# Kernel optimization log

Hardware: AMD Instinct MI355X
Metric: run time of the kernel (lower is better)

Reference implementation:

```python
import jax, jax.numpy as jnp
import numpy as np


def setup_inputs() -> dict:
    key = jax.random.key(0)
    ks = jax.random.split(key, 4)
    B, L, E = 2, 2048, 512
    scale = 0.02
    return {
        "x": jax.random.normal(ks[0], (B, L, E), dtype=jnp.float32),
        "Wq": jax.random.normal(ks[1], (E, E), dtype=jnp.float32) * scale,
        "bq": jnp.zeros((E,), dtype=jnp.float32),
        "Wk": jax.random.normal(ks[2], (E, E), dtype=jnp.float32) * scale,
        "bk": jnp.zeros((E,), dtype=jnp.float32),
        "Wv": jax.random.normal(ks[3], (E, E), dtype=jnp.float32) * scale,
        "bv": jnp.zeros((E,), dtype=jnp.float32),
        "window_size": 64,
    }


def reference(x, Wq, bq, Wk, bk, Wv, bv, window_size):
    # x: [B, L, E]; Linear weights stored torch-style as [out, in].
    B, L, E = x.shape
    q = jnp.einsum("ble,fe->blf", x, Wq) + bq  # [B, L, E]
    k = jnp.einsum("ble,fe->blf", x, Wk) + bk
    v = jnp.einsum("ble,fe->blf", x, Wv) + bv

    w = window_size
    W = 2 * w + 1
    # Window indices per query position i: [i-w, i+w], clipped; invalid masked.
    offsets = jnp.arange(-w, w + 1)                 # [W]
    idx = jnp.arange(L)[:, None] + offsets[None, :]  # [L, W]
    valid = (idx >= 0) & (idx < L)                   # [L, W]
    idx_c = jnp.clip(idx, 0, L - 1)

    k_win = k[:, idx_c]  # [B, L, W, E]
    v_win = v[:, idx_c]  # [B, L, W, E]

    scores = jnp.einsum("ble,blwe->blw", q, k_win) / jnp.sqrt(jnp.float32(E))
    scores = jnp.where(valid[None, :, :], scores, -jnp.inf)
    probs = jax.nn.softmax(scores, axis=-1)          # [B, L, W]
    out = jnp.einsum("blw,blwe->ble", probs, v_win)  # [B, L, E]
    return out
```

## Files before the change

kernel.cpp:

```cpp
#include <hip/hip_runtime.h>
#include <cstdint>
#include <cstddef>

#define L_SEQ 2048
#define E_DIM 512
#define B_SZ 2
#define WIN 64
#define SCALE_QK 0.044194173824159216f

typedef __attribute__((ext_vector_type(8))) short short8;
typedef __attribute__((ext_vector_type(4))) float floatx4;

__device__ __forceinline__ unsigned short f2bf(float f) {
    unsigned int u = __float_as_uint(f);
    u += 0x7FFFu + ((u >> 16) & 1u);
    return (unsigned short)(u >> 16);
}

__device__ __forceinline__ uint4 pk8(const float4 lo, const float4 hi) {
    uint4 r;
    asm("v_cvt_pk_bf16_f32 %0, %1, %2" : "=v"(r.x) : "v"(lo.x), "v"(lo.y));
    asm("v_cvt_pk_bf16_f32 %0, %1, %2" : "=v"(r.y) : "v"(lo.z), "v"(lo.w));
    asm("v_cvt_pk_bf16_f32 %0, %1, %2" : "=v"(r.z) : "v"(hi.x), "v"(hi.y));
    asm("v_cvt_pk_bf16_f32 %0, %1, %2" : "=v"(r.w) : "v"(hi.z), "v"(hi.w));
    return r;
}

__device__ __forceinline__ void ld16cvt(const float* g, uint4& r0, uint4& r1) {
    float4 f0 = *(const float4*)(g);
    float4 f1 = *(const float4*)(g + 4);
    float4 f2 = *(const float4*)(g + 8);
    float4 f3 = *(const float4*)(g + 12);
    r0 = pk8(f0, f1);
    r1 = pk8(f2, f3);
}

#define ALD 72
__global__ __launch_bounds__(256, 2) void qkv_fused(
    const float* __restrict__ x,
    const float* __restrict__ Wq, const float* __restrict__ Wk, const float* __restrict__ Wv,
    const float* __restrict__ bq, const float* __restrict__ bk, const float* __restrict__ bv,
    unsigned short* __restrict__ q, unsigned short* __restrict__ k,
    unsigned short* __restrict__ vt)
{
    __shared__ __align__(16) unsigned short As[64 * ALD];
    __shared__ __align__(16) unsigned short Bs[3][64 * ALD];

    const int t = threadIdx.x;
    const int w = t >> 6, l = t & 63;
    const int m0 = blockIdx.x * 64, n0 = blockIdx.y * 64;
    const float* Ws[3] = { Wq, Wk, Wv };

    floatx4 acc[3][2][2] = {};
    const int wm = (w >> 1) * 32, wn = (w & 1) * 32;
    const int fr = l & 15, fq = l >> 4, fk = fq * 8;

    const int srow = t >> 2, scol = (t & 3) * 16;
    const float* gA = x + (size_t)(m0 + srow) * 512 + scol;

    float bv_[3][2];
    {
        const float* bs[3] = { bq, bk, bv };
#pragma unroll
        for (int z = 0; z < 3; z++)
#pragma unroll
            for (int j = 0; j < 2; j++) bv_[z][j] = bs[z][n0 + wn + j * 16 + fr];
    }

    for (int kt = 0; kt < 8; kt++) {
        const int kk = kt * 64;
        uint4 r0, r1;
        ld16cvt(gA + kk, r0, r1);
        *(uint4*)&As[srow * ALD + scol]     = r0;
        *(uint4*)&As[srow * ALD + scol + 8] = r1;
#pragma unroll
        for (int z = 0; z < 3; z++) {
            ld16cvt(Ws[z] + (size_t)(n0 + srow) * 512 + scol + kk, r0, r1);
            *(uint4*)&Bs[z][srow * ALD + scol]     = r0;
            *(uint4*)&Bs[z][srow * ALD + scol + 8] = r1;
        }
        __syncthreads();

        short8 a[2][2];
#pragma unroll
        for (int i = 0; i < 2; i++)
#pragma unroll
            for (int kh = 0; kh < 2; kh++)
                a[i][kh] = *(const short8*)&As[(wm + i * 16 + fr) * ALD + kh * 32 + fk];
#pragma unroll
        for (int z = 0; z < 3; z++) {
            short8 bf[2][2];
#pragma unroll
            for (int j = 0; j < 2; j++)
#pragma unroll
                for (int kh = 0; kh < 2; kh++)
                    bf[j][kh] = *(const short8*)&Bs[z][(wn + j * 16 + fr) * ALD + kh * 32 + fk];
#pragma unroll
            for (int kh = 0; kh < 2; kh++)
#pragma unroll
                for (int i = 0; i < 2; i++)
#pragma unroll
                    for (int j = 0; j < 2; j++)
                        acc[z][i][j] = __builtin_amdgcn_mfma_f32_16x16x32_bf16(a[i][kh], bf[j][kh], acc[z][i][j], 0, 0, 0);
        }
        __syncthreads();
    }

    unsigned short* Tl = As;
    const int tr = t >> 2, tc = (t & 3) * 16;
#pragma unroll
    for (int z = 0; z < 3; z++) {
        if (z) __syncthreads();
        if (z < 2) {
#pragma unroll
            for (int i = 0; i < 2; i++)
#pragma unroll
                for (int j = 0; j < 2; j++)
#pragma unroll
                    for (int r = 0; r < 4; r++)
                        Tl[(wm + i * 16 + fq * 4 + r) * ALD + wn + j * 16 + fr] =
                            f2bf(acc[z][i][j][r] + bv_[z][j]);
        } else {
#pragma unroll
            for (int i = 0; i < 2; i++)
#pragma unroll
                for (int j = 0; j < 2; j++)
#pragma unroll
                    for (int r = 0; r < 4; r++)
                        Tl[(wn + j * 16 + fr) * ALD + wm + i * 16 + fq * 4 + r] =
                            f2bf(acc[z][i][j][r] + bv_[z][j]);
        }
        __syncthreads();

        uint4 v0 = *(const uint4*)&Tl[tr * ALD + tc];
        uint4 v1 = *(const uint4*)&Tl[tr * ALD + tc + 8];
        if (z < 2) {
            unsigned short* out = (z == 0) ? q : k;
            *(uint4*)&out[(size_t)(m0 + tr) * 512 + n0 + tc]     = v0;
            *(uint4*)&out[(size_t)(m0 + tr) * 512 + n0 + tc + 8] = v1;
        } else {
            *(uint4*)&vt[(size_t)(n0 + tr) * 4096 + m0 + tc]     = v0;
            *(uint4*)&vt[(size_t)(n0 + tr) * 4096 + m0 + tc + 8] = v1;
        }
    }
}

#define SLD 164
__global__ __launch_bounds__(512) void attn_fused(
    const unsigned short* __restrict__ qb, const unsigned short* __restrict__ kb,
    const unsigned short* __restrict__ vt, float* __restrict__ out)
{
    __shared__ __align__(16) float Sl[16 * SLD];

    const int t = threadIdx.x;
    const int w = t >> 6, l = t & 63;
    const int fr = l & 15, fq = l >> 4;
    const int bx = blockIdx.x;
    const int Qt = (bx & 7) * 16 + (bx >> 3);
    const int Q0 = Qt * 16;
    const int b  = blockIdx.y;
    const int R0 = Q0 - WIN;

    {
        const unsigned short* qrow = qb + (size_t)(b * L_SEQ + Q0 + fr) * 512 + fq * 8;
        short8 qf[16];
#pragma unroll
        for (int ks = 0; ks < 16; ks++) qf[ks] = *(const short8*)(qrow + ks * 32);

        for (int nt = w; nt < 9; nt += 8) {
            const int tok = R0 + nt * 16 + fr;
            const bool kvalid = (tok >= 0) && (tok < L_SEQ);
            const int tokc = min(max(tok, 0), L_SEQ - 1);
            const unsigned short* krow = kb + (size_t)(b * L_SEQ + tokc) * 512 + fq * 8;

            floatx4 acc0 = {}, acc1 = {};
            short8 bfr[8];
#pragma unroll
            for (int ks = 0; ks < 8; ks++) bfr[ks] = *(const short8*)(krow + ks * 32);
#pragma unroll
            for (int ks = 0; ks < 8; ks++)
                acc0 = __builtin_amdgcn_mfma_f32_16x16x32_bf16(qf[ks], bfr[ks], acc0, 0, 0, 0);
#pragma unroll
            for (int ks = 0; ks < 8; ks++) bfr[ks] = *(const short8*)(krow + (8 + ks) * 32);
#pragma unroll
            for (int ks = 0; ks < 8; ks++)
                acc1 = __builtin_amdgcn_mfma_f32_16x16x32_bf16(qf[8 + ks], bfr[ks], acc1, 0, 0, 0);

            const int jg = nt * 16 + fr;
#pragma unroll
            for (int r = 0; r < 4; r++) {
                int qq = fq * 4 + r;
                bool valid = kvalid && (jg >= qq) && (jg <= qq + 128);
                Sl[qq * SLD + jg] = valid ? (acc0[r] + acc1[r]) * SCALE_QK : -1e30f;
            }
        }
    }
    __syncthreads();

    const float* Srow = &Sl[fr * SLD + fq * 8];
    float sv[5][8];
#pragma unroll
    for (int ks = 0; ks < 5; ks++) {
        float4 u0 = *(const float4*)(Srow + ks * 32);
        float4 u1 = *(const float4*)(Srow + ks * 32 + 4);
        sv[ks][0] = u0.x; sv[ks][1] = u0.y; sv[ks][2] = u0.z; sv[ks][3] = u0.w;
        sv[ks][4] = u1.x; sv[ks][5] = u1.y; sv[ks][6] = u1.z; sv[ks][7] = u1.w;
    }
    if (fq >= 2) {
#pragma unroll
        for (int j = 0; j < 8; j++) sv[4][j] = -1e30f;
    }
    float m = -1e30f;
#pragma unroll
    for (int ks = 0; ks < 5; ks++)
#pragma unroll
        for (int j = 0; j < 8; j++) m = fmaxf(m, sv[ks][j]);
    m = fmaxf(m, __shfl_xor(m, 16));
    m = fmaxf(m, __shfl_xor(m, 32));
    float sum = 0.f;
#pragma unroll
    for (int ks = 0; ks < 5; ks++)
#pragma unroll
        for (int j = 0; j < 8; j++) { float e = __expf(sv[ks][j] - m); sv[ks][j] = e; sum += e; }
    sum += __shfl_xor(sum, 16);
    sum += __shfl_xor(sum, 32);
    float inv = 1.f / sum;

    short8 a[5];
#pragma unroll
    for (int ks = 0; ks < 5; ks++)
#pragma unroll
        for (int j = 0; j < 8; j++) a[ks][j] = (short)f2bf(sv[ks][j] * inv);

    const int EC = w * 64;
    int tkc[5];
#pragma unroll
    for (int ks = 0; ks < 5; ks++) {
        int tok0 = R0 + ks * 32 + fq * 8;
        tkc[ks] = min(max(tok0, 0), L_SEQ - 8);
    }
    floatx4 oa[4] = {};
#pragma unroll
    for (int et = 0; et < 4; et++) {
        const unsigned short* vrow = vt + (size_t)(EC + et * 16 + fr) * 4096 + b * L_SEQ;
        short8 vfr[5];
#pragma unroll
        for (int ks = 0; ks < 5; ks++) vfr[ks] = *(const short8*)(vrow + tkc[ks]);
#pragma unroll
        for (int ks = 0; ks < 5; ks++)
            oa[et] = __builtin_amdgcn_mfma_f32_16x16x32_bf16(a[ks], vfr[ks], oa[et], 0, 0, 0);
    }

    float* op = out + (size_t)b * L_SEQ * E_DIM;
#pragma unroll
    for (int et = 0; et < 4; et++)
#pragma unroll
        for (int r = 0; r < 4; r++)
            op[(size_t)(Q0 + fq * 4 + r) * 512 + EC + et * 16 + fr] = oa[et][r];
}

extern "C" void kernel_launch(void* const* d_in, const int* in_sizes, int n_in,
                              void* d_out, int out_size, void* d_ws, size_t ws_size,
                              hipStream_t stream)
{
    const float* x  = (const float*)d_in[0];
    const float* Wq = (const float*)d_in[1];
    const float* bq = (const float*)d_in[2];
    const float* Wk = (const float*)d_in[3];
    const float* bk = (const float*)d_in[4];
    const float* Wv = (const float*)d_in[5];
    const float* bv = (const float*)d_in[6];
    float* out = (float*)d_out;

    char* ws = (char*)d_ws;
    unsigned short* qb = (unsigned short*)(ws);
    unsigned short* kb = (unsigned short*)(ws + 4194304);
    unsigned short* vt = (unsigned short*)(ws + 8388608);

    qkv_fused<<<dim3(64, 8), 256, 0, stream>>>(x, Wq, Wk, Wv, bq, bk, bv, qb, kb, vt);
    attn_fused<<<dim3(128, 2), 512, 0, stream>>>(qb, kb, vt, out);
}
```

Before: 112.0 us.

## Merge QKV projection and attention into one persistent kernel with grid barriers

```diff
diff --git a/kernel.cpp b/kernel.cpp
--- a/kernel.cpp
+++ b/kernel.cpp
@@ -4,9 +4,11 @@
 
 #define L_SEQ 2048
 #define E_DIM 512
-#define B_SZ 2
 #define WIN 64
 #define SCALE_QK 0.044194173824159216f
+
+#define NBLK 512
+#define NTHR 256
 
 typedef __attribute__((ext_vector_type(8))) short short8;
 typedef __attribute__((ext_vector_type(4))) float floatx4;
@@ -17,246 +19,269 @@
     return (unsigned short)(u >> 16);
 }
 
-__device__ __forceinline__ uint4 pk8(const float4 lo, const float4 hi) {
-    uint4 r;
-    asm("v_cvt_pk_bf16_f32 %0, %1, %2" : "=v"(r.x) : "v"(lo.x), "v"(lo.y));
-    asm("v_cvt_pk_bf16_f32 %0, %1, %2" : "=v"(r.y) : "v"(lo.z), "v"(lo.w));
-    asm("v_cvt_pk_bf16_f32 %0, %1, %2" : "=v"(r.z) : "v"(hi.x), "v"(hi.y));
-    asm("v_cvt_pk_bf16_f32 %0, %1, %2" : "=v"(r.w) : "v"(hi.z), "v"(hi.w));
-    return r;
-}
-
-__device__ __forceinline__ void ld16cvt(const float* g, uint4& r0, uint4& r1) {
-    float4 f0 = *(const float4*)(g);
-    float4 f1 = *(const float4*)(g + 4);
-    float4 f2 = *(const float4*)(g + 8);
-    float4 f3 = *(const float4*)(g + 12);
-    r0 = pk8(f0, f1);
-    r1 = pk8(f2, f3);
-}
-
-#define ALD 72
-__global__ __launch_bounds__(256, 2) void qkv_fused(
-    const float* __restrict__ x,
-    const float* __restrict__ Wq, const float* __restrict__ Wk, const float* __restrict__ Wv,
-    const float* __restrict__ bq, const float* __restrict__ bk, const float* __restrict__ bv,
-    unsigned short* __restrict__ q, unsigned short* __restrict__ k,
-    unsigned short* __restrict__ vt)
-{
-    __shared__ __align__(16) unsigned short As[64 * ALD];
-    __shared__ __align__(16) unsigned short Bs[3][64 * ALD];
-
-    const int t = threadIdx.x;
-    const int w = t >> 6, l = t & 63;
-    const int m0 = blockIdx.x * 64, n0 = blockIdx.y * 64;
-    const float* Ws[3] = { Wq, Wk, Wv };
-
-    floatx4 acc[3][2][2] = {};
-    const int wm = (w >> 1) * 32, wn = (w & 1) * 32;
-    const int fr = l & 15, fq = l >> 4, fk = fq * 8;
-
-    const int srow = t >> 2, scol = (t & 3) * 16;
-    const float* gA = x + (size_t)(m0 + srow) * 512 + scol;
-
-    float bv_[3][2];
-    {
-        const float* bs[3] = { bq, bk, bv };
-#pragma unroll
-        for (int z = 0; z < 3; z++)
-#pragma unroll
-            for (int j = 0; j < 2; j++) bv_[z][j] = bs[z][n0 + wn + j * 16 + fr];
-    }
-
-    for (int kt = 0; kt < 8; kt++) {
-        const int kk = kt * 64;
-        uint4 r0, r1;
-        ld16cvt(gA + kk, r0, r1);
-        *(uint4*)&As[srow * ALD + scol]     = r0;
-        *(uint4*)&As[srow * ALD + scol + 8] = r1;
-#pragma unroll
-        for (int z = 0; z < 3; z++) {
-            ld16cvt(Ws[z] + (size_t)(n0 + srow) * 512 + scol + kk, r0, r1);
-            *(uint4*)&Bs[z][srow * ALD + scol]     = r0;
-            *(uint4*)&Bs[z][srow * ALD + scol + 8] = r1;
-        }
-        __syncthreads();
-
-        short8 a[2][2];
-#pragma unroll
-        for (int i = 0; i < 2; i++)
-#pragma unroll
-            for (int kh = 0; kh < 2; kh++)
-                a[i][kh] = *(const short8*)&As[(wm + i * 16 + fr) * ALD + kh * 32 + fk];
-#pragma unroll
-        for (int z = 0; z < 3; z++) {
-            short8 bf[2][2];
-#pragma unroll
-            for (int j = 0; j < 2; j++)
-#pragma unroll
-                for (int kh = 0; kh < 2; kh++)
-                    bf[j][kh] = *(const short8*)&Bs[z][(wn + j * 16 + fr) * ALD + kh * 32 + fk];
-#pragma unroll
-            for (int kh = 0; kh < 2; kh++)
-#pragma unroll
-                for (int i = 0; i < 2; i++)
-#pragma unroll
-                    for (int j = 0; j < 2; j++)
-                        acc[z][i][j] = __builtin_amdgcn_mfma_f32_16x16x32_bf16(a[i][kh], bf[j][kh], acc[z][i][j], 0, 0, 0);
-        }
-        __syncthreads();
-    }
-
-    unsigned short* Tl = As;
-    const int tr = t >> 2, tc = (t & 3) * 16;
-#pragma unroll
-    for (int z = 0; z < 3; z++) {
-        if (z) __syncthreads();
-        if (z < 2) {
-#pragma unroll
-            for (int i = 0; i < 2; i++)
-#pragma unroll
-                for (int j = 0; j < 2; j++)
-#pragma unroll
-                    for (int r = 0; r < 4; r++)
-                        Tl[(wm + i * 16 + fq * 4 + r) * ALD + wn + j * 16 + fr] =
-                            f2bf(acc[z][i][j][r] + bv_[z][j]);
-        } else {
-#pragma unroll
-            for (int i = 0; i < 2; i++)
-#pragma unroll
-                for (int j = 0; j < 2; j++)
-#pragma unroll
-                    for (int r = 0; r < 4; r++)
-                        Tl[(wn + j * 16 + fr) * ALD + wm + i * 16 + fq * 4 + r] =
-                            f2bf(acc[z][i][j][r] + bv_[z][j]);
-        }
-        __syncthreads();
-
-        uint4 v0 = *(const uint4*)&Tl[tr * ALD + tc];
-        uint4 v1 = *(const uint4*)&Tl[tr * ALD + tc + 8];
-        if (z < 2) {
-            unsigned short* out = (z == 0) ? q : k;
-            *(uint4*)&out[(size_t)(m0 + tr) * 512 + n0 + tc]     = v0;
-            *(uint4*)&out[(size_t)(m0 + tr) * 512 + n0 + tc + 8] = v1;
-        } else {
-            *(uint4*)&vt[(size_t)(n0 + tr) * 4096 + m0 + tc]     = v0;
-            *(uint4*)&vt[(size_t)(n0 + tr) * 4096 + m0 + tc + 8] = v1;
-        }
-    }
-}
-
-#define SLD 164
-__global__ __launch_bounds__(512) void attn_fused(
-    const unsigned short* __restrict__ qb, const unsigned short* __restrict__ kb,
-    const unsigned short* __restrict__ vt, float* __restrict__ out)
-{
-    __shared__ __align__(16) float Sl[16 * SLD];
-
-    const int t = threadIdx.x;
-    const int w = t >> 6, l = t & 63;
-    const int fr = l & 15, fq = l >> 4;
-    const int bx = blockIdx.x;
-    const int Qt = (bx & 7) * 16 + (bx >> 3);
-    const int Q0 = Qt * 16;
-    const int b  = blockIdx.y;
-    const int R0 = Q0 - WIN;
-
-    {
-        const unsigned short* qrow = qb + (size_t)(b * L_SEQ + Q0 + fr) * 512 + fq * 8;
-        short8 qf[16];
-#pragma unroll
-        for (int ks = 0; ks < 16; ks++) qf[ks] = *(const short8*)(qrow + ks * 32);
-
-        for (int nt = w; nt < 9; nt += 8) {
-            const int tok = R0 + nt * 16 + fr;
-            const bool kvalid = (tok >= 0) && (tok < L_SEQ);
-            const int tokc = min(max(tok, 0), L_SEQ - 1);
-            const unsigned short* krow = kb + (size_t)(b * L_SEQ + tokc) * 512 + fq * 8;
-
-            floatx4 acc0 = {}, acc1 = {};
-            short8 bfr[8];
-#pragma unroll
-            for (int ks = 0; ks < 8; ks++) bfr[ks] = *(const short8*)(krow + ks * 32);
-#pragma unroll
-            for (int ks = 0; ks < 8; ks++)
-                acc0 = __builtin_amdgcn_mfma_f32_16x16x32_bf16(qf[ks], bfr[ks], acc0, 0, 0, 0);
-#pragma unroll
-            for (int ks = 0; ks < 8; ks++) bfr[ks] = *(const short8*)(krow + (8 + ks) * 32);
-#pragma unroll
-            for (int ks = 0; ks < 8; ks++)
-                acc1 = __builtin_amdgcn_mfma_f32_16x16x32_bf16(qf[8 + ks], bfr[ks], acc1, 0, 0, 0);
-
-            const int jg = nt * 16 + fr;
-#pragma unroll
-            for (int r = 0; r < 4; r++) {
-                int qq = fq * 4 + r;
-                bool valid = kvalid && (jg >= qq) && (jg <= qq + 128);
-                Sl[qq * SLD + jg] = valid ? (acc0[r] + acc1[r]) * SCALE_QK : -1e30f;
-            }
-        }
+__device__ __forceinline__ void gbar(unsigned int* cnt, unsigned int target) {
+    __syncthreads();
+    if (threadIdx.x == 0) {
+        __threadfence();
+        __hip_atomic_fetch_add(cnt, 1u, __ATOMIC_ACQ_REL, __HIP_MEMORY_SCOPE_AGENT);
+        unsigned int v = __hip_atomic_load(cnt, __ATOMIC_ACQUIRE, __HIP_MEMORY_SCOPE_AGENT);
+        for (int it = 0; it < 4000000 && v < target; ++it) {
+            __builtin_amdgcn_s_sleep(8);
+            v = __hip_atomic_load(cnt, __ATOMIC_ACQUIRE, __HIP_MEMORY_SCOPE_AGENT);
+        }
+        __threadfence();
     }
     __syncthreads();
-
-    const float* Srow = &Sl[fr * SLD + fq * 8];
-    float sv[5][8];
-#pragma unroll
-    for (int ks = 0; ks < 5; ks++) {
-        float4 u0 = *(const float4*)(Srow + ks * 32);
-        float4 u1 = *(const float4*)(Srow + ks * 32 + 4);
-        sv[ks][0] = u0.x; sv[ks][1] = u0.y; sv[ks][2] = u0.z; sv[ks][3] = u0.w;
-        sv[ks][4] = u1.x; sv[ks][5] = u1.y; sv[ks][6] = u1.z; sv[ks][7] = u1.w;
+}
+
+#define ALD 72
+#define SLD 164
+__global__ __launch_bounds__(256, 2) void mega(
+    const float* __restrict__ x,
+    const float* __restrict__ Wq, const float* __restrict__ bq,
+    const float* __restrict__ Wk, const float* __restrict__ bk,
+    const float* __restrict__ Wv, const float* __restrict__ bv,
+    float* __restrict__ out,
+    unsigned short* __restrict__ xb, unsigned short* __restrict__ wb,
+    unsigned short* __restrict__ qb, unsigned short* __restrict__ kb,
+    unsigned short* __restrict__ vt, unsigned int* __restrict__ cnt)
+{
+    __shared__ __align__(16) char lds_raw[36864];
+
+    const int t   = threadIdx.x;
+    const int bid = blockIdx.x;
+
+    for (long i = (long)bid * NTHR + t; i < 720896; i += (long)NBLK * NTHR) {
+        const float* src; unsigned short* dst; long off;
+        if (i < 524288) {
+            src = x; dst = xb; off = i;
+        } else {
+            long j = i - 524288;
+            int wsel = (int)(j >> 16);
+            off = j & 65535;
+            src = (wsel == 0) ? Wq : ((wsel == 1) ? Wk : Wv);
+            dst = wb + (long)wsel * 262144;
+        }
+        float4 f = ((const float4*)src)[off];
+        ushort4 o;
+        o.x = f2bf(f.x); o.y = f2bf(f.y); o.z = f2bf(f.z); o.w = f2bf(f.w);
+        ((ushort4*)dst)[off] = o;
     }
-    if (fq >= 2) {
-#pragma unroll
-        for (int j = 0; j < 8; j++) sv[4][j] = -1e30f;
+    gbar(cnt, NBLK);
+
+    {
+        const int mt = bid & 63, nt = bid >> 6;
+        const int m0 = mt * 64, n0 = nt * 64;
+
+        unsigned short* As = (unsigned short*)lds_raw;
+        unsigned short* Bs = As + 64 * ALD;
+
+        const int w = t >> 6, l = t & 63;
+        const int wm = (w >> 1) * 32, wn = (w & 1) * 32;
+        const int fr = l & 15, fq = l >> 4, fk = fq * 8;
+
+        const int srow = t >> 2, scol = (t & 3) * 16;
+        const unsigned short* gA = xb + (size_t)(m0 + srow) * 512 + scol;
+        const unsigned short* gB = wb + (size_t)(n0 + srow) * 512 + scol;
+
+        float bv_[3][2];
+        {
+            const float* bs[3] = { bq, bk, bv };
+#pragma unroll
+            for (int z = 0; z < 3; z++)
+#pragma unroll
+                for (int j = 0; j < 2; j++) bv_[z][j] = bs[z][n0 + wn + j * 16 + fr];
+        }
+
+        floatx4 acc[3][2][2] = {};
+
+        for (int kt = 0; kt < 8; kt++) {
+            const int kk = kt * 64;
+            *(uint4*)&As[srow * ALD + scol]     = *(const uint4*)(gA + kk);
+            *(uint4*)&As[srow * ALD + scol + 8] = *(const uint4*)(gA + kk + 8);
+#pragma unroll
+            for (int z = 0; z < 3; z++) {
+                *(uint4*)&Bs[z * 64 * ALD + srow * ALD + scol]     = *(const uint4*)(gB + (size_t)z * 262144 + kk);
+                *(uint4*)&Bs[z * 64 * ALD + srow * ALD + scol + 8] = *(const uint4*)(gB + (size_t)z * 262144 + kk + 8);
+            }
+            __syncthreads();
+
+            short8 a[2][2];
+#pragma unroll
+            for (int i = 0; i < 2; i++)
+#pragma unroll
+                for (int kh = 0; kh < 2; kh++)
+                    a[i][kh] = *(const short8*)&As[(wm + i * 16 + fr) * ALD + kh * 32 + fk];
+#pragma unroll
+            for (int z = 0; z < 3; z++) {
+                short8 bf[2][2];
+#pragma unroll
+                for (int j = 0; j < 2; j++)
+#pragma unroll
+                    for (int kh = 0; kh < 2; kh++)
+                        bf[j][kh] = *(const short8*)&Bs[z * 64 * ALD + (wn + j * 16 + fr) * ALD + kh * 32 + fk];
+#pragma unroll
+                for (int kh = 0; kh < 2; kh++)
+#pragma unroll
+                    for (int i = 0; i < 2; i++)
+#pragma unroll
+                        for (int j = 0; j < 2; j++)
+                            acc[z][i][j] = __builtin_amdgcn_mfma_f32_16x16x32_bf16(a[i][kh], bf[j][kh], acc[z][i][j], 0, 0, 0);
+            }
+            __syncthreads();
+        }
+
+        unsigned short* Tl = As;
+        const int tr = t >> 2, tc = (t & 3) * 16;
+#pragma unroll
+        for (int z = 0; z < 3; z++) {
+            if (z) __syncthreads();
+            if (z < 2) {
+#pragma unroll
+                for (int i = 0; i < 2; i++)
+#pragma unroll
+                    for (int j = 0; j < 2; j++)
+#pragma unroll
+                        for (int r = 0; r < 4; r++)
+                            Tl[(wm + i * 16 + fq * 4 + r) * ALD + wn + j * 16 + fr] =
+                                f2bf(acc[z][i][j][r] + bv_[z][j]);
+            } else {
+#pragma unroll
+                for (int i = 0; i < 2; i++)
+#pragma unroll
+                    for (int j = 0; j < 2; j++)
+#pragma unroll
+                        for (int r = 0; r < 4; r++)
+                            Tl[(wn + j * 16 + fr) * ALD + wm + i * 16 + fq * 4 + r] =
+                                f2bf(acc[z][i][j][r] + bv_[z][j]);
+            }
+            __syncthreads();
+
+            uint4 v0 = *(const uint4*)&Tl[tr * ALD + tc];
+            uint4 v1 = *(const uint4*)&Tl[tr * ALD + tc + 8];
+            if (z < 2) {
+                unsigned short* o = (z == 0) ? qb : kb;
+                size_t off = (size_t)(m0 + tr) * 512 + n0 + tc;
+                *(uint4*)&o[off]     = v0;
+                *(uint4*)&o[off + 8] = v1;
+            } else {
+                size_t off = (size_t)(n0 + tr) * 4096 + m0 + tc;
+                *(uint4*)&vt[off]     = v0;
+                *(uint4*)&vt[off + 8] = v1;
+            }
+        }
     }
-    float m = -1e30f;
-#pragma unroll
-    for (int ks = 0; ks < 5; ks++)
-#pragma unroll
-        for (int j = 0; j < 8; j++) m = fmaxf(m, sv[ks][j]);
-    m = fmaxf(m, __shfl_xor(m, 16));
-    m = fmaxf(m, __shfl_xor(m, 32));
-    float sum = 0.f;
-#pragma unroll
-    for (int ks = 0; ks < 5; ks++)
-#pragma unroll
-        for (int j = 0; j < 8; j++) { float e = __expf(sv[ks][j] - m); sv[ks][j] = e; sum += e; }
-    sum += __shfl_xor(sum, 16);
-    sum += __shfl_xor(sum, 32);
-    float inv = 1.f / sum;
-
-    short8 a[5];
-#pragma unroll
-    for (int ks = 0; ks < 5; ks++)
-#pragma unroll
-        for (int j = 0; j < 8; j++) a[ks][j] = (short)f2bf(sv[ks][j] * inv);
-
-    const int EC = w * 64;
-    int tkc[5];
-#pragma unroll
-    for (int ks = 0; ks < 5; ks++) {
-        int tok0 = R0 + ks * 32 + fq * 8;
-        tkc[ks] = min(max(tok0, 0), L_SEQ - 8);
+    gbar(cnt, 2 * NBLK);
+
+    {
+        float* Sl = (float*)lds_raw;
+
+        const int g   = bid >> 3, xcd = bid & 7;
+        const int Qt  = xcd * 16 + (g & 15);
+        const int eh  = (g >> 4) & 1;
+        const int b   = g >> 5;
+        const int w = t >> 6, l = t & 63;
+        const int fr = l & 15, fq = l >> 4;
+        const int Q0 = Qt * 16;
+        const int R0 = Q0 - WIN;
+
+        {
+            const unsigned short* qrow = qb + (size_t)(b * L_SEQ + Q0 + fr) * 512 + fq * 8;
+            short8 qf[16];
+#pragma unroll
+            for (int ks = 0; ks < 16; ks++) qf[ks] = *(const short8*)(qrow + ks * 32);
+
+            for (int nt = w; nt < 9; nt += 4) {
+                const int tok = R0 + nt * 16 + fr;
+                const bool kvalid = (tok >= 0) && (tok < L_SEQ);
+                const int tokc = min(max(tok, 0), L_SEQ - 1);
+                const unsigned short* krow = kb + (size_t)(b * L_SEQ + tokc) * 512 + fq * 8;
+
+                floatx4 acc0 = {}, acc1 = {};
+                short8 bfr[8];
+#pragma unroll
+                for (int ks = 0; ks < 8; ks++) bfr[ks] = *(const short8*)(krow + ks * 32);
+#pragma unroll
+                for (int ks = 0; ks < 8; ks++)
+                    acc0 = __builtin_amdgcn_mfma_f32_16x16x32_bf16(qf[ks], bfr[ks], acc0, 0, 0, 0);
+#pragma unroll
+                for (int ks = 0; ks < 8; ks++) bfr[ks] = *(const short8*)(krow + (8 + ks) * 32);
+#pragma unroll
+                for (int ks = 0; ks < 8; ks++)
+                    acc1 = __builtin_amdgcn_mfma_f32_16x16x32_bf16(qf[8 + ks], bfr[ks], acc1, 0, 0, 0);
+
+                const int jg = nt * 16 + fr;
+#pragma unroll
+                for (int r = 0; r < 4; r++) {
+                    int qq = fq * 4 + r;
+                    bool valid = kvalid && (jg >= qq) && (jg <= qq + 128);
+                    Sl[qq * SLD + jg] = valid ? (acc0[r] + acc1[r]) * SCALE_QK : -1e30f;
+                }
+            }
+        }
+        __syncthreads();
+
+        const float* Srow = &Sl[fr * SLD + fq * 8];
+        float sv[5][8];
+#pragma unroll
+        for (int ks = 0; ks < 5; ks++) {
+            float4 u0 = *(const float4*)(Srow + ks * 32);
+            float4 u1 = *(const float4*)(Srow + ks * 32 + 4);
+            sv[ks][0] = u0.x; sv[ks][1] = u0.y; sv[ks][2] = u0.z; sv[ks][3] = u0.w;
+            sv[ks][4] = u1.x; sv[ks][5] = u1.y; sv[ks][6] = u1.z; sv[ks][7] = u1.w;
+        }
+        if (fq >= 2) {
+#pragma unroll
+            for (int j = 0; j < 8; j++) sv[4][j] = -1e30f;
+        }
+        float m = -1e30f;
+#pragma unroll
+        for (int ks = 0; ks < 5; ks++)
+#pragma unroll
+            for (int j = 0; j < 8; j++) m = fmaxf(m, sv[ks][j]);
+        m = fmaxf(m, __shfl_xor(m, 16));
+        m = fmaxf(m, __shfl_xor(m, 32));
+        float sum = 0.f;
+#pragma unroll
+        for (int ks = 0; ks < 5; ks++)
+#pragma unroll
+            for (int j = 0; j < 8; j++) { float e = __expf(sv[ks][j] - m); sv[ks][j] = e; sum += e; }
+        sum += __shfl_xor(sum, 16);
+        sum += __shfl_xor(sum, 32);
+        float inv = 1.f / sum;
+
+        short8 a[5];
+#pragma unroll
+        for (int ks = 0; ks < 5; ks++)
+#pragma unroll
+            for (int j = 0; j < 8; j++) a[ks][j] = (short)f2bf(sv[ks][j] * inv);
+
+        const int EC = eh * 256 + w * 64;
+        int tkc[5];
+#pragma unroll
+        for (int ks = 0; ks < 5; ks++) {
+            int tok0 = R0 + ks * 32 + fq * 8;
+            tkc[ks] = min(max(tok0, 0), L_SEQ - 8);
+        }
+        floatx4 oa[4] = {};
+#pragma unroll
+        for (int et = 0; et < 4; et++) {
+            const unsigned short* vrow = vt + (size_t)(EC + et * 16 + fr) * 4096 + b * L_SEQ;
+            short8 vfr[5];
+#pragma unroll
+            for (int ks = 0; ks < 5; ks++) vfr[ks] = *(const short8*)(vrow + tkc[ks]);
+#pragma unroll
+            for (int ks = 0; ks < 5; ks++)
+                oa[et] = __builtin_amdgcn_mfma_f32_16x16x32_bf16(a[ks], vfr[ks], oa[et], 0, 0, 0);
+        }
+
+        float* op = out + (size_t)b * L_SEQ * E_DIM;
+#pragma unroll
+        for (int et = 0; et < 4; et++)
+#pragma unroll
+            for (int r = 0; r < 4; r++)
+                op[(size_t)(Q0 + fq * 4 + r) * 512 + EC + et * 16 + fr] = oa[et][r];
     }
-    floatx4 oa[4] = {};
-#pragma unroll
-    for (int et = 0; et < 4; et++) {
-        const unsigned short* vrow = vt + (size_t)(EC + et * 16 + fr) * 4096 + b * L_SEQ;
-        short8 vfr[5];
-#pragma unroll
-        for (int ks = 0; ks < 5; ks++) vfr[ks] = *(const short8*)(vrow + tkc[ks]);
-#pragma unroll
-        for (int ks = 0; ks < 5; ks++)
-            oa[et] = __builtin_amdgcn_mfma_f32_16x16x32_bf16(a[ks], vfr[ks], oa[et], 0, 0, 0);
-    }
-
-    float* op = out + (size_t)b * L_SEQ * E_DIM;
-#pragma unroll
-    for (int et = 0; et < 4; et++)
-#pragma unroll
-        for (int r = 0; r < 4; r++)
-            op[(size_t)(Q0 + fq * 4 + r) * 512 + EC + et * 16 + fr] = oa[et][r];
 }
 
 extern "C" void kernel_launch(void* const* d_in, const int* in_sizes, int n_in,
@@ -276,7 +301,11 @@
     unsigned short* qb = (unsigned short*)(ws);
     unsigned short* kb = (unsigned short*)(ws + 4194304);
     unsigned short* vt = (unsigned short*)(ws + 8388608);
-
-    qkv_fused<<<dim3(64, 8), 256, 0, stream>>>(x, Wq, Wk, Wv, bq, bk, bv, qb, kb, vt);
-    attn_fused<<<dim3(128, 2), 512, 0, stream>>>(qb, kb, vt, out);
+    unsigned short* xb = (unsigned short*)(ws + 12582912);
+    unsigned short* wb = (unsigned short*)(ws + 16777216);
+    unsigned int*  cnt = (unsigned int*)(ws + 33554432);
+
+    hipMemsetAsync(cnt, 0, 64, stream);
+    mega<<<NBLK, NTHR, 0, stream>>>(x, Wq, bq, Wk, bk, Wv, bv, out,
+                                    xb, wb, qb, kb, vt, cnt);
 }
```

Result: slower. 206.2 us (+84.1%).

## Pre-convert inputs to bf16 in separate kernel and split attention over E halves

Applied to the files above, without the earlier changes.

```diff
diff --git a/kernel.cpp b/kernel.cpp
--- a/kernel.cpp
+++ b/kernel.cpp
@@ -4,7 +4,6 @@
 
 #define L_SEQ 2048
 #define E_DIM 512
-#define B_SZ 2
 #define WIN 64
 #define SCALE_QK 0.044194173824159216f
 
@@ -17,28 +16,33 @@
     return (unsigned short)(u >> 16);
 }
 
-__device__ __forceinline__ uint4 pk8(const float4 lo, const float4 hi) {
-    uint4 r;
-    asm("v_cvt_pk_bf16_f32 %0, %1, %2" : "=v"(r.x) : "v"(lo.x), "v"(lo.y));
-    asm("v_cvt_pk_bf16_f32 %0, %1, %2" : "=v"(r.y) : "v"(lo.z), "v"(lo.w));
-    asm("v_cvt_pk_bf16_f32 %0, %1, %2" : "=v"(r.z) : "v"(hi.x), "v"(hi.y));
-    asm("v_cvt_pk_bf16_f32 %0, %1, %2" : "=v"(r.w) : "v"(hi.z), "v"(hi.w));
-    return r;
-}
-
-__device__ __forceinline__ void ld16cvt(const float* g, uint4& r0, uint4& r1) {
-    float4 f0 = *(const float4*)(g);
-    float4 f1 = *(const float4*)(g + 4);
-    float4 f2 = *(const float4*)(g + 8);
-    float4 f3 = *(const float4*)(g + 12);
-    r0 = pk8(f0, f1);
-    r1 = pk8(f2, f3);
+__global__ __launch_bounds__(256) void cvt_kernel(
+    const float* __restrict__ x, const float* __restrict__ wq,
+    const float* __restrict__ wk, const float* __restrict__ wv,
+    unsigned short* __restrict__ xb, unsigned short* __restrict__ wb)
+{
+    long i = (long)blockIdx.x * 256 + threadIdx.x;
+    const float* src;
+    unsigned short* dst;
+    long off;
+    if (i < 524288) {
+        src = x; dst = xb; off = i;
+    } else {
+        long j = i - 524288;
+        int w = (int)(j >> 16);
+        off = j & 65535;
+        src = (w == 0) ? wq : ((w == 1) ? wk : wv);
+        dst = wb + (long)w * 262144;
+    }
+    float4 f = ((const float4*)src)[off];
+    ushort4 o;
+    o.x = f2bf(f.x); o.y = f2bf(f.y); o.z = f2bf(f.z); o.w = f2bf(f.w);
+    ((ushort4*)dst)[off] = o;
 }
 
 #define ALD 72
-__global__ __launch_bounds__(256, 2) void qkv_fused(
-    const float* __restrict__ x,
-    const float* __restrict__ Wq, const float* __restrict__ Wk, const float* __restrict__ Wv,
+__global__ __launch_bounds__(256, 2) void qkv_zloop(
+    const unsigned short* __restrict__ xb, const unsigned short* __restrict__ wb,
     const float* __restrict__ bq, const float* __restrict__ bk, const float* __restrict__ bv,
     unsigned short* __restrict__ q, unsigned short* __restrict__ k,
     unsigned short* __restrict__ vt)
@@ -47,16 +51,17 @@
     __shared__ __align__(16) unsigned short Bs[3][64 * ALD];
 
     const int t = threadIdx.x;
+    const int bid = blockIdx.x;
+    const int mt = bid & 63, nt = bid >> 6;
+    const int m0 = mt * 64, n0 = nt * 64;
+
     const int w = t >> 6, l = t & 63;
-    const int m0 = blockIdx.x * 64, n0 = blockIdx.y * 64;
-    const float* Ws[3] = { Wq, Wk, Wv };
-
-    floatx4 acc[3][2][2] = {};
     const int wm = (w >> 1) * 32, wn = (w & 1) * 32;
     const int fr = l & 15, fq = l >> 4, fk = fq * 8;
 
     const int srow = t >> 2, scol = (t & 3) * 16;
-    const float* gA = x + (size_t)(m0 + srow) * 512 + scol;
+    const unsigned short* gA = xb + (size_t)(m0 + srow) * 512 + scol;
+    const unsigned short* gB = wb + (size_t)(n0 + srow) * 512 + scol;
 
     float bv_[3][2];
     {
@@ -67,17 +72,16 @@
             for (int j = 0; j < 2; j++) bv_[z][j] = bs[z][n0 + wn + j * 16 + fr];
     }
 
+    floatx4 acc[3][2][2] = {};
+
     for (int kt = 0; kt < 8; kt++) {
         const int kk = kt * 64;
-        uint4 r0, r1;
-        ld16cvt(gA + kk, r0, r1);
-        *(uint4*)&As[srow * ALD + scol]     = r0;
-        *(uint4*)&As[srow * ALD + scol + 8] = r1;
+        *(uint4*)&As[srow * ALD + scol]     = *(const uint4*)(gA + kk);
+        *(uint4*)&As[srow * ALD + scol + 8] = *(const uint4*)(gA + kk + 8);
 #pragma unroll
         for (int z = 0; z < 3; z++) {
-            ld16cvt(Ws[z] + (size_t)(n0 + srow) * 512 + scol + kk, r0, r1);
-            *(uint4*)&Bs[z][srow * ALD + scol]     = r0;
-            *(uint4*)&Bs[z][srow * ALD + scol + 8] = r1;
+            *(uint4*)&Bs[z][srow * ALD + scol]     = *(const uint4*)(gB + (size_t)z * 262144 + kk);
+            *(uint4*)&Bs[z][srow * ALD + scol + 8] = *(const uint4*)(gB + (size_t)z * 262144 + kk + 8);
         }
         __syncthreads();
 
@@ -135,18 +139,20 @@
         uint4 v0 = *(const uint4*)&Tl[tr * ALD + tc];
         uint4 v1 = *(const uint4*)&Tl[tr * ALD + tc + 8];
         if (z < 2) {
-            unsigned short* out = (z == 0) ? q : k;
-            *(uint4*)&out[(size_t)(m0 + tr) * 512 + n0 + tc]     = v0;
-            *(uint4*)&out[(size_t)(m0 + tr) * 512 + n0 + tc + 8] = v1;
+            unsigned short* o = (z == 0) ? q : k;
+            size_t off = (size_t)(m0 + tr) * 512 + n0 + tc;
+            *(uint4*)&o[off]     = v0;
+            *(uint4*)&o[off + 8] = v1;
         } else {
-            *(uint4*)&vt[(size_t)(n0 + tr) * 4096 + m0 + tc]     = v0;
-            *(uint4*)&vt[(size_t)(n0 + tr) * 4096 + m0 + tc + 8] = v1;
+            size_t off = (size_t)(n0 + tr) * 4096 + m0 + tc;
+            *(uint4*)&vt[off]     = v0;
+            *(uint4*)&vt[off + 8] = v1;
         }
     }
 }
 
 #define SLD 164
-__global__ __launch_bounds__(512) void attn_fused(
+__global__ __launch_bounds__(512, 4) void attn_fused(
     const unsigned short* __restrict__ qb, const unsigned short* __restrict__ kb,
     const unsigned short* __restrict__ vt, float* __restrict__ out)
 {
@@ -159,6 +165,7 @@
     const int Qt = (bx & 7) * 16 + (bx >> 3);
     const int Q0 = Qt * 16;
     const int b  = blockIdx.y;
+    const int eh = blockIdx.z;
     const int R0 = Q0 - WIN;
 
     {
@@ -232,16 +239,16 @@
 #pragma unroll
         for (int j = 0; j < 8; j++) a[ks][j] = (short)f2bf(sv[ks][j] * inv);
 
-    const int EC = w * 64;
+    const int EC = eh * 256 + w * 32;
     int tkc[5];
 #pragma unroll
     for (int ks = 0; ks < 5; ks++) {
         int tok0 = R0 + ks * 32 + fq * 8;
         tkc[ks] = min(max(tok0, 0), L_SEQ - 8);
     }
-    floatx4 oa[4] = {};
-#pragma unroll
-    for (int et = 0; et < 4; et++) {
+    floatx4 oa[2] = {};
+#pragma unroll
+    for (int et = 0; et < 2; et++) {
         const unsigned short* vrow = vt + (size_t)(EC + et * 16 + fr) * 4096 + b * L_SEQ;
         short8 vfr[5];
 #pragma unroll
@@ -253,7 +260,7 @@
 
     float* op = out + (size_t)b * L_SEQ * E_DIM;
 #pragma unroll
-    for (int et = 0; et < 4; et++)
+    for (int et = 0; et < 2; et++)
 #pragma unroll
         for (int r = 0; r < 4; r++)
             op[(size_t)(Q0 + fq * 4 + r) * 512 + EC + et * 16 + fr] = oa[et][r];
@@ -276,7 +283,10 @@
     unsigned short* qb = (unsigned short*)(ws);
     unsigned short* kb = (unsigned short*)(ws + 4194304);
     unsigned short* vt = (unsigned short*)(ws + 8388608);
-
-    qkv_fused<<<dim3(64, 8), 256, 0, stream>>>(x, Wq, Wk, Wv, bq, bk, bv, qb, kb, vt);
-    attn_fused<<<dim3(128, 2), 512, 0, stream>>>(qb, kb, vt, out);
-}
+    unsigned short* xb = (unsigned short*)(ws + 12582912);
+    unsigned short* wb = (unsigned short*)(ws + 16777216);
+
+    cvt_kernel<<<2816, 256, 0, stream>>>(x, Wq, Wk, Wv, xb, wb);
+    qkv_zloop<<<512, 256, 0, stream>>>(xb, wb, bq, bk, bv, qb, kb, vt);
+    attn_fused<<<dim3(128, 2, 2), 512, 0, stream>>>(qb, kb, vt, out);
+}
```

Measured after the change: 118.8 us. 6.1% more time.
